# Kernel optimization log

Hardware: AMD Instinct MI355X
Metric: run time of the kernel (lower is better)

## Reference

```python
import jax, jax.numpy as jnp
import numpy as np

BN_EPS = 1e-5
N_NODES, N_EDGES, D_IN, HID = 100000, 1600000, 64, 128


def _bn(x, g, b, m, v):
    # BatchNorm1d in eval mode: running stats
    return (x - m) * jax.lax.rsqrt(v + BN_EPS) * g + b


def _gin_agg(x, edge_index, eps):
    # PyG GINConv aggregation: out[dst] = (1+eps)*x[dst] + sum_{src->dst} x[src]
    src, dst = edge_index[0], edge_index[1]
    s = jax.ops.segment_sum(x[src], dst, num_segments=x.shape[0])
    return (1.0 + eps) * x + s


def setup_inputs() -> dict:
    key = jax.random.key(0)
    ks = jax.random.split(key, 24)
    sc = 0.05
    d = {
        'x': jax.random.normal(ks[0], (N_NODES, D_IN), dtype=jnp.float32),
        'edge_index': jax.random.randint(ks[1], (2, N_EDGES), 0, N_NODES, dtype=jnp.int64),
        'eps1': jnp.zeros((), jnp.float32),
        'W1a': jax.random.normal(ks[2], (D_IN, HID), jnp.float32) * sc,
        'b1a': jnp.zeros((HID,), jnp.float32),
        'W1b': jax.random.normal(ks[3], (HID, HID), jnp.float32) * sc,
        'b1b': jnp.zeros((HID,), jnp.float32),
        'g1': jnp.ones((HID,), jnp.float32), 'be1': jnp.zeros((HID,), jnp.float32),
        'm1': jnp.zeros((HID,), jnp.float32), 'v1': jnp.ones((HID,), jnp.float32),
        'eps2': jnp.zeros((), jnp.float32),
        'W2a': jax.random.normal(ks[4], (HID, HID), jnp.float32) * sc,
        'b2a': jnp.zeros((HID,), jnp.float32),
        'g2': jnp.ones((HID,), jnp.float32), 'be2': jnp.zeros((HID,), jnp.float32),
        'm2': jnp.zeros((HID,), jnp.float32), 'v2': jnp.ones((HID,), jnp.float32),
        'eps3': jnp.zeros((), jnp.float32),
        'W3a': jax.random.normal(ks[5], (HID, HID), jnp.float32) * sc,
        'b3a': jnp.zeros((HID,), jnp.float32),
        'W3b': jax.random.normal(ks[6], (HID, HID), jnp.float32) * sc,
        'b3b': jnp.zeros((HID,), jnp.float32),
        'g3': jnp.ones((HID,), jnp.float32), 'be3': jnp.zeros((HID,), jnp.float32),
        'm3': jnp.zeros((HID,), jnp.float32), 'v3': jnp.ones((HID,), jnp.float32),
        'Wl': jax.random.normal(ks[7], (HID, HID), jnp.float32) * sc,
        'bl': jnp.zeros((HID,), jnp.float32),
        'Wf': jax.random.normal(ks[8], (HID, 1), jnp.float32) * sc,
        'bf': jnp.zeros((1,), jnp.float32),
    }
    return d


def reference(x, edge_index, eps1, W1a, b1a, W1b, b1b, g1, be1, m1, v1,
              eps2, W2a, b2a, g2, be2, m2, v2,
              eps3, W3a, b3a, W3b, b3b, g3, be3, m3, v3,
              Wl, bl, Wf, bf):
    # GINConv 1: agg -> Linear(64,128) ReLU -> Linear(128,128) ReLU -> BN
    h = _gin_agg(x, edge_index, eps1)
    h = jax.nn.relu(h @ W1a + b1a)
    h = jax.nn.relu(h @ W1b + b1b)
    h = _bn(h, g1, be1, m1, v1)
    # GINConv 2: agg -> Linear ReLU -> BN
    h = _gin_agg(h, edge_index, eps2)
    h = jax.nn.relu(h @ W2a + b2a)
    h = _bn(h, g2, be2, m2, v2)
    # GINConv 3: agg -> Linear ReLU -> Linear ReLU -> BN
    h = _gin_agg(h, edge_index, eps3)
    h = jax.nn.relu(h @ W3a + b3a)
    h = jax.nn.relu(h @ W3b + b3b)
    h = _bn(h, g3, be3, m3, v3)
    # head: lin1 + ReLU (dropout identity in eval), fc, squeeze
    h = jax.nn.relu(h @ Wl + bl)
    out = (h @ Wf + bf).squeeze(-1)  # [N]
    return out
```

## Files before the change

kernel.cpp:

```cpp
#include <hip/hip_runtime.h>


constexpr int NN  = 100000;
constexpr int NE  = 1600000;
constexpr int DIN = 64;
constexpr int HID = 128;

constexpr int BSH   = 9;
constexpr int NBUCK = 196;
constexpr int NBLK  = 200;
constexpr int CHUNK = 8000;

typedef __attribute__((ext_vector_type(4))) float f32x4;
typedef __attribute__((ext_vector_type(8))) short bf16x8;
typedef __attribute__((ext_vector_type(8))) unsigned short u16x8;

__device__ __forceinline__ short f2bf(float f) {
    union { float f; unsigned u; } x; x.f = f;
    unsigned r = x.u + 0x7fffu + ((x.u >> 16) & 1u);
    return (short)(r >> 16);
}
__device__ __forceinline__ float bf2f(short s) {
    union { unsigned u; float f; } x; x.u = ((unsigned)(unsigned short)s) << 16;
    return x.f;
}

__device__ __forceinline__ void wave_lds_fence() {
    __builtin_amdgcn_sched_barrier(0);
    asm volatile("s_waitcnt lgkmcnt(0)" ::: "memory");
    __builtin_amdgcn_sched_barrier(0);
}

__global__ __launch_bounds__(256)
void bhist_kernel(const int* __restrict__ eidx, int* __restrict__ bcnt,
                  int* __restrict__ pbase) {
    __shared__ int lh[NBUCK];
    int b = blockIdx.x;
    for (int i = threadIdx.x; i < NBUCK; i += 256) lh[i] = 0;
    __syncthreads();
    int e0 = b * CHUNK;
    for (int i = threadIdx.x; i < CHUNK; i += 256)
        atomicAdd(&lh[eidx[NE + e0 + i] >> BSH], 1);
    __syncthreads();
    for (int i = threadIdx.x; i < NBUCK; i += 256)
        pbase[b * NBUCK + i] = atomicAdd(&bcnt[i], lh[i]);
}

__global__ void bscan_kernel(const int* __restrict__ bcnt, int* __restrict__ bbase,
                             int* __restrict__ offs) {
    __shared__ int lds[256];
    int t = threadIdx.x;
    int v = (t < NBUCK) ? bcnt[t] : 0;
    lds[t] = v; __syncthreads();
    #pragma unroll
    for (int o = 1; o < 256; o <<= 1) {
        int x = (t >= o) ? lds[t - o] : 0;
        __syncthreads();
        lds[t] += x;
        __syncthreads();
    }
    if (t < NBUCK) bbase[t] = lds[t] - v;
    if (t == 0) { bbase[NBUCK] = NE; offs[NN] = NE; }
}

__global__ __launch_bounds__(256)
void part_kernel(const int* __restrict__ eidx, const int* __restrict__ bbase,
                 const int* __restrict__ pbase, int2* __restrict__ tmp) {
    __shared__ int lh[NBUCK], lofs[NBUCK], lcnt[NBUCK], gb[NBUCK];
    __shared__ int sb[256];
    __shared__ int2 lp[CHUNK];
    int b = blockIdx.x;
    int t = threadIdx.x;
    for (int i = t; i < NBUCK; i += 256) { lh[i] = 0; lcnt[i] = 0; }
    __syncthreads();
    int e0 = b * CHUNK;
    for (int i = t; i < CHUNK; i += 256)
        atomicAdd(&lh[eidx[NE + e0 + i] >> BSH], 1);
    __syncthreads();
    {
        int v = (t < NBUCK) ? lh[t] : 0;
        sb[t] = v; __syncthreads();
        #pragma unroll
        for (int o = 1; o < 256; o <<= 1) {
            int x = (t >= o) ? sb[t - o] : 0;
            __syncthreads();
            sb[t] += x;
            __syncthreads();
        }
        if (t < NBUCK) {
            lofs[t] = sb[t] - v;
            gb[t]   = bbase[t] + pbase[b * NBUCK + t];
        }
    }
    __syncthreads();
    for (int i = t; i < CHUNK; i += 256) {
        int s = eidx[e0 + i], d = eidx[NE + e0 + i];
        int bk = d >> BSH;
        int r = atomicAdd(&lcnt[bk], 1);
        lp[lofs[bk] + r] = int2{s, d};
    }
    __syncthreads();
    for (int i = t; i < CHUNK; i += 256) {
        int2 p = lp[i];
        int bk = p.y >> BSH;
        tmp[gb[bk] + (i - lofs[bk])] = p;
    }
}

__global__ __launch_bounds__(512)
void bsort_kernel(const int* __restrict__ bbase, const int2* __restrict__ tmp,
                  int* __restrict__ offs, int* __restrict__ esrc) {
    __shared__ int h[512], lo[512], cnt[512];
    int bk = blockIdx.x;
    int n0 = bk << BSH;
    int lo0 = bbase[bk], hi0 = bbase[bk + 1];
    int t = threadIdx.x;
    h[t] = 0; cnt[t] = 0;
    __syncthreads();
    for (int i = lo0 + t; i < hi0; i += 512)
        atomicAdd(&h[tmp[i].y - n0], 1);
    __syncthreads();
    int v = h[t];
    lo[t] = v; __syncthreads();
    #pragma unroll
    for (int o = 1; o < 512; o <<= 1) {
        int x = (t >= o) ? lo[t - o] : 0;
        __syncthreads();
        lo[t] += x;
        __syncthreads();
    }
    int excl = lo[t] - v;
    __syncthreads();
    lo[t] = excl;
    __syncthreads();
    if (n0 + t < NN) offs[n0 + t] = lo0 + excl;
    for (int i = lo0 + t; i < hi0; i += 512) {
        int2 p = tmp[i];
        int ld = p.y - n0;
        int r = atomicAdd(&cnt[ld], 1);
        esrc[lo0 + lo[ld] + r] = p.x;
    }
}

__global__ void cvt_kernel(const float* __restrict__ x, unsigned short* __restrict__ xb) {
    int i = blockIdx.x * 256 + threadIdx.x;
    if (i >= NN * DIN / 8) return;
    const f32x4* p = (const f32x4*)x + (size_t)i * 2;
    f32x4 v0 = p[0], v1 = p[1];
    u16x8 o;
    #pragma unroll
    for (int j = 0; j < 4; ++j) {
        o[j]     = (unsigned short)f2bf(v0[j]);
        o[j + 4] = (unsigned short)f2bf(v1[j]);
    }
    ((u16x8*)xb)[i] = o;
}

template<int D>
__global__ __launch_bounds__(256)
void aggb_kernel(const float* __restrict__ hf, const unsigned short* __restrict__ hb,
                 const int* __restrict__ offs, const int* __restrict__ esrc,
                 const float* __restrict__ epsp, float* __restrict__ out) {
    constexpr int TPN = D / 8;
    int node = blockIdx.x * (256 / TPN) + threadIdx.x / TPN;
    int f    = threadIdx.x % TPN;
    if (node >= NN) return;
    const u16x8* h8 = (const u16x8*)hb;
    float eps = 1.0f + *epsp;

    const float* hrow = hf + (size_t)node * D + f * 8;
    f32x4 a0 = *(const f32x4*)hrow * eps;
    f32x4 a1 = *(const f32x4*)(hrow + 4) * eps;
    f32x4 b0 = (f32x4)0.f, b1 = (f32x4)0.f;

    union { unsigned u; float fv; } cvt;
    auto acc8 = [&](u16x8 t, f32x4& x0, f32x4& x1) {
        #pragma unroll
        for (int j = 0; j < 4; ++j) { cvt.u = ((unsigned)t[j]) << 16;     x0[j] += cvt.fv; }
        #pragma unroll
        for (int j = 0; j < 4; ++j) { cvt.u = ((unsigned)t[j + 4]) << 16; x1[j] += cvt.fv; }
    };

    int k = offs[node], k1 = offs[node + 1];
    for (; k + 8 <= k1; k += 8) {
        int s0 = esrc[k+0], s1 = esrc[k+1], s2 = esrc[k+2], s3 = esrc[k+3];
        int s4 = esrc[k+4], s5 = esrc[k+5], s6 = esrc[k+6], s7 = esrc[k+7];
        u16x8 t0 = h8[(size_t)s0*TPN+f], t1 = h8[(size_t)s1*TPN+f];
        u16x8 t2 = h8[(size_t)s2*TPN+f], t3 = h8[(size_t)s3*TPN+f];
        u16x8 t4 = h8[(size_t)s4*TPN+f], t5 = h8[(size_t)s5*TPN+f];
        u16x8 t6 = h8[(size_t)s6*TPN+f], t7 = h8[(size_t)s7*TPN+f];
        acc8(t0, a0, a1); acc8(t1, b0, b1); acc8(t2, a0, a1); acc8(t3, b0, b1);
        acc8(t4, a0, a1); acc8(t5, b0, b1); acc8(t6, a0, a1); acc8(t7, b0, b1);
    }
    for (; k + 2 <= k1; k += 2) {
        u16x8 t0 = h8[(size_t)esrc[k]*TPN+f];
        u16x8 t1 = h8[(size_t)esrc[k+1]*TPN+f];
        acc8(t0, a0, a1); acc8(t1, b0, b1);
    }
    if (k < k1) acc8(h8[(size_t)esrc[k]*TPN+f], a0, a1);

    float* orow = out + (size_t)node * D + f * 8;
    *(f32x4*)orow       = a0 + b0;
    *(f32x4*)(orow + 4) = a1 + b1;
}

__global__ void packall_kernel(const float* __restrict__ W1a, const float* __restrict__ W1b,
                               const float* __restrict__ W2a, const float* __restrict__ W3a,
                               const float* __restrict__ W3b, const float* __restrict__ Wl,
                               short* P1a, short* P1b, short* P2a,
                               short* P3a, short* P3b, short* Pl) {
    const float* W; short* P; int K;
    switch (blockIdx.y) {
        case 0: W = W1a; P = P1a; K = 64;  break;
        case 1: W = W1b; P = P1b; K = 128; break;
        case 2: W = W2a; P = P2a; K = 128; break;
        case 3: W = W3a; P = P3a; K = 128; break;
        case 4: W = W3b; P = P3b; K = 128; break;
        default: W = Wl; P = Pl;  K = 128; break;
    }
    int T = (K / 32) * 8 * 64;
    int idx = blockIdx.x * 256 + threadIdx.x;
    if (idx >= T) return;
    int c  = idx >> 9;
    int nt = (idx >> 6) & 7;
    int l  = idx & 63;
    int col   = nt * 16 + (l & 15);
    int kbase = c * 32 + (l >> 4) * 8;
    bf16x8 hi, lo;
    #pragma unroll
    for (int j = 0; j < 8; ++j) {
        float w = W[(kbase + j) * HID + col];
        short h = f2bf(w);
        hi[j] = h;
        lo[j] = f2bf(w - bf2f(h));
    }
    *(bf16x8*)&P[(size_t)idx * 8]       = hi;
    *(bf16x8*)&P[(size_t)(T + idx) * 8] = lo;
}

__global__ __launch_bounds__(512)
void gemm_bn_kernel(const float* __restrict__ A, const short* __restrict__ P,
                    const float* __restrict__ bias,
                    const float* __restrict__ g, const float* __restrict__ be,
                    const float* __restrict__ m, const float* __restrict__ v,
                    float* __restrict__ out, unsigned short* __restrict__ hbout, int M) {
    constexpr int NCH = 4;
    constexpr int T   = NCH * 8 * 64;
    __shared__ short wlds[2 * T * 8];

    const int tid  = threadIdx.x;
    const int wid  = tid >> 6;
    const int lane = tid & 63;

    for (int i = tid; i < 2 * T; i += 512)
        ((bf16x8*)wlds)[i] = ((const bf16x8*)P)[i];
    __syncthreads();

    const int rlo  = lane & 15;
    const int kgrp = lane >> 4;
    const int row  = blockIdx.x * 128 + wid * 16 + rlo;
    const int r    = row < M ? row : M - 1;
    const float* arow = A + (size_t)r * 128 + kgrp * 8;

    f32x4 acc[8];
    #pragma unroll
    for (int i = 0; i < 8; ++i) acc[i] = (f32x4)0.0f;

    #pragma unroll
    for (int c = 0; c < NCH; ++c) {
        f32x4 a0 = *(const f32x4*)(arow + c * 32);
        f32x4 a1 = *(const f32x4*)(arow + c * 32 + 4);
        bf16x8 ah, al;
        #pragma unroll
        for (int j = 0; j < 4; ++j) {
            short h0 = f2bf(a0[j]);
            short h1 = f2bf(a1[j]);
            ah[j]     = h0;
            ah[j + 4] = h1;
            al[j]     = f2bf(a0[j] - bf2f(h0));
            al[j + 4] = f2bf(a1[j] - bf2f(h1));
        }
        #pragma unroll
        for (int nt = 0; nt < 8; ++nt) {
            int fi = ((c * 8) + nt) * 64 + lane;
            bf16x8 wh = *(bf16x8*)&wlds[(size_t)fi * 8];
            bf16x8 wl = *(bf16x8*)&wlds[(size_t)(T + fi) * 8];
            acc[nt] = __builtin_amdgcn_mfma_f32_16x16x32_bf16(ah, wh, acc[nt], 0, 0, 0);
            acc[nt] = __builtin_amdgcn_mfma_f32_16x16x32_bf16(al, wh, acc[nt], 0, 0, 0);
            acc[nt] = __builtin_amdgcn_mfma_f32_16x16x32_bf16(ah, wl, acc[nt], 0, 0, 0);
        }
    }

    #pragma unroll
    for (int nt = 0; nt < 8; ++nt) {
        int col  = nt * 16 + rlo;
        float bb = bias[col];
        float sv = g[col] * rsqrtf(v[col] + 1e-5f);
        float tv = be[col] - m[col] * sv;
        #pragma unroll
        for (int jj = 0; jj < 4; ++jj) {
            int rr = blockIdx.x * 128 + wid * 16 + kgrp * 4 + jj;
            float val = fmaxf(acc[nt][jj] + bb, 0.f) * sv + tv;
            if (rr < M) {
                out[(size_t)rr * 128 + col] = val;
                hbout[(size_t)rr * 128 + col] = (unsigned short)f2bf(val);
            }
        }
    }
}

template<int K1>
__global__ __launch_bounds__(128)
void fused2_kernel(const float* __restrict__ A,
                   const short* __restrict__ P1, const float* __restrict__ bias1,
                   const short* __restrict__ P2, const float* __restrict__ bias2,
                   const float* __restrict__ g, const float* __restrict__ be,
                   const float* __restrict__ m, const float* __restrict__ v,
                   float* __restrict__ out, unsigned short* __restrict__ hbout, int M) {
    constexpr int NCH1 = K1 / 32;
    constexpr int T1   = NCH1 * 8 * 64;
    constexpr int T2   = 4 * 8 * 64;
    constexpr int LDW  = 136;
    __shared__ short h1hi[64 * LDW];
    __shared__ short h1lo[64 * LDW];

    const int tid  = threadIdx.x;
    const int wid  = tid >> 6;
    const int lane = tid & 63;
    const int rlo  = lane & 15;
    const int kgrp = lane >> 4;

    const int rowA = blockIdx.x * 64 + wid * 16 + rlo;
    const int rowB = rowA + 32;
    const int rA   = rowA < M ? rowA : M - 1;
    const int rB   = rowB < M ? rowB : M - 1;
    const float* arowA = A + (size_t)rA * K1 + kgrp * 8;
    const float* arowB = A + (size_t)rB * K1 + kgrp * 8;

    const bf16x8* P1v = (const bf16x8*)P1;
    const bf16x8* P2v = (const bf16x8*)P2;

    f32x4 accA[8], accB[8];
    #pragma unroll
    for (int i = 0; i < 8; ++i) { accA[i] = (f32x4)0.0f; accB[i] = (f32x4)0.0f; }

    #pragma unroll
    for (int c = 0; c < NCH1; ++c) {
        f32x4 aA0 = *(const f32x4*)(arowA + c * 32);
        f32x4 aA1 = *(const f32x4*)(arowA + c * 32 + 4);
        f32x4 aB0 = *(const f32x4*)(arowB + c * 32);
        f32x4 aB1 = *(const f32x4*)(arowB + c * 32 + 4);
        bf16x8 ahA, alA, ahB, alB;
        #pragma unroll
        for (int j = 0; j < 4; ++j) {
            short h;
            h = f2bf(aA0[j]); ahA[j]   = h; alA[j]   = f2bf(aA0[j] - bf2f(h));
            h = f2bf(aA1[j]); ahA[j+4] = h; alA[j+4] = f2bf(aA1[j] - bf2f(h));
            h = f2bf(aB0[j]); ahB[j]   = h; alB[j]   = f2bf(aB0[j] - bf2f(h));
            h = f2bf(aB1[j]); ahB[j+4] = h; alB[j+4] = f2bf(aB1[j] - bf2f(h));
        }
        #pragma unroll
        for (int nt = 0; nt < 8; ++nt) {
            int fi = ((c * 8) + nt) * 64 + lane;
            bf16x8 wh = P1v[fi];
            bf16x8 wl = P1v[T1 + fi];
            accA[nt] = __builtin_amdgcn_mfma_f32_16x16x32_bf16(ahA, wh, accA[nt], 0, 0, 0);
            accA[nt] = __builtin_amdgcn_mfma_f32_16x16x32_bf16(alA, wh, accA[nt], 0, 0, 0);
            accA[nt] = __builtin_amdgcn_mfma_f32_16x16x32_bf16(ahA, wl, accA[nt], 0, 0, 0);
            accB[nt] = __builtin_amdgcn_mfma_f32_16x16x32_bf16(ahB, wh, accB[nt], 0, 0, 0);
            accB[nt] = __builtin_amdgcn_mfma_f32_16x16x32_bf16(alB, wh, accB[nt], 0, 0, 0);
            accB[nt] = __builtin_amdgcn_mfma_f32_16x16x32_bf16(ahB, wl, accB[nt], 0, 0, 0);
        }
    }

    #pragma unroll
    for (int nt = 0; nt < 8; ++nt) {
        int col  = nt * 16 + rlo;
        float bb = bias1[col];
        #pragma unroll
        for (int jj = 0; jj < 4; ++jj) {
            int lrA = wid * 16 + kgrp * 4 + jj;
            float vA = fmaxf(accA[nt][jj] + bb, 0.f);
            short hA = f2bf(vA);
            h1hi[lrA * LDW + col] = hA;
            h1lo[lrA * LDW + col] = f2bf(vA - bf2f(hA));
            int lrB = lrA + 32;
            float vB = fmaxf(accB[nt][jj] + bb, 0.f);
            short hB = f2bf(vB);
            h1hi[lrB * LDW + col] = hB;
            h1lo[lrB * LDW + col] = f2bf(vB - bf2f(hB));
        }
    }
    wave_lds_fence();

    #pragma unroll
    for (int i = 0; i < 8; ++i) { accA[i] = (f32x4)0.0f; accB[i] = (f32x4)0.0f; }
    const int lrA2 = wid * 16 + rlo;
    const int lrB2 = lrA2 + 32;
    #pragma unroll
    for (int c = 0; c < 4; ++c) {
        bf16x8 ahA = *(bf16x8*)&h1hi[lrA2 * LDW + c * 32 + kgrp * 8];
        bf16x8 alA = *(bf16x8*)&h1lo[lrA2 * LDW + c * 32 + kgrp * 8];
        bf16x8 ahB = *(bf16x8*)&h1hi[lrB2 * LDW + c * 32 + kgrp * 8];
        bf16x8 alB = *(bf16x8*)&h1lo[lrB2 * LDW + c * 32 + kgrp * 8];
        #pragma unroll
        for (int nt = 0; nt < 8; ++nt) {
            int fi = ((c * 8) + nt) * 64 + lane;
            bf16x8 wh = P2v[fi];
            bf16x8 wl = P2v[T2 + fi];
            accA[nt] = __builtin_amdgcn_mfma_f32_16x16x32_bf16(ahA, wh, accA[nt], 0, 0, 0);
            accA[nt] = __builtin_amdgcn_mfma_f32_16x16x32_bf16(alA, wh, accA[nt], 0, 0, 0);
            accA[nt] = __builtin_amdgcn_mfma_f32_16x16x32_bf16(ahA, wl, accA[nt], 0, 0, 0);
            accB[nt] = __builtin_amdgcn_mfma_f32_16x16x32_bf16(ahB, wh, accB[nt], 0, 0, 0);
            accB[nt] = __builtin_amdgcn_mfma_f32_16x16x32_bf16(alB, wh, accB[nt], 0, 0, 0);
            accB[nt] = __builtin_amdgcn_mfma_f32_16x16x32_bf16(ahB, wl, accB[nt], 0, 0, 0);
        }
    }

    #pragma unroll
    for (int nt = 0; nt < 8; ++nt) {
        int col  = nt * 16 + rlo;
        float bb = bias2[col];
        float sv = g[col] * rsqrtf(v[col] + 1e-5f);
        float tv = be[col] - m[col] * sv;
        #pragma unroll
        for (int jj = 0; jj < 4; ++jj) {
            int rrA = blockIdx.x * 64 + wid * 16 + kgrp * 4 + jj;
            float vA = fmaxf(accA[nt][jj] + bb, 0.f) * sv + tv;
            if (rrA < M) {
                out[(size_t)rrA * 128 + col] = vA;
                hbout[(size_t)rrA * 128 + col] = (unsigned short)f2bf(vA);
            }
            int rrB = rrA + 32;
            float vB = fmaxf(accB[nt][jj] + bb, 0.f) * sv + tv;
            if (rrB < M) {
                out[(size_t)rrB * 128 + col] = vB;
                hbout[(size_t)rrB * 128 + col] = (unsigned short)f2bf(vB);
            }
        }
    }
}

__global__ __launch_bounds__(128)
void fused3_kernel(const float* __restrict__ A,
                   const short* __restrict__ P1, const float* __restrict__ bias1,
                   const short* __restrict__ P2, const float* __restrict__ bias2,
                   const float* __restrict__ g, const float* __restrict__ be,
                   const float* __restrict__ m, const float* __restrict__ v,
                   const short* __restrict__ Pl, const float* __restrict__ bl,
                   const float* __restrict__ Wf, const float* __restrict__ bf,
                   float* __restrict__ out, int M) {
    constexpr int T  = 4 * 8 * 64;
    constexpr int LDW = 136;
    __shared__ short h1hi[64 * LDW];
    __shared__ short h1lo[64 * LDW];

    const int tid  = threadIdx.x;
    const int wid  = tid >> 6;
    const int lane = tid & 63;
    const int rlo  = lane & 15;
    const int kgrp = lane >> 4;

    const int rowA = blockIdx.x * 64 + wid * 16 + rlo;
    const int rowB = rowA + 32;
    const int rA   = rowA < M ? rowA : M - 1;
    const int rB   = rowB < M ? rowB : M - 1;
    const float* arowA = A + (size_t)rA * 128 + kgrp * 8;
    const float* arowB = A + (size_t)rB * 128 + kgrp * 8;

    const bf16x8* P1v = (const bf16x8*)P1;
    const bf16x8* P2v = (const bf16x8*)P2;
    const bf16x8* Plv = (const bf16x8*)Pl;

    f32x4 accA[8], accB[8];
    #pragma unroll
    for (int i = 0; i < 8; ++i) { accA[i] = (f32x4)0.0f; accB[i] = (f32x4)0.0f; }

    #pragma unroll
    for (int c = 0; c < 4; ++c) {
        f32x4 aA0 = *(const f32x4*)(arowA + c * 32);
        f32x4 aA1 = *(const f32x4*)(arowA + c * 32 + 4);
        f32x4 aB0 = *(const f32x4*)(arowB + c * 32);
        f32x4 aB1 = *(const f32x4*)(arowB + c * 32 + 4);
        bf16x8 ahA, alA, ahB, alB;
        #pragma unroll
        for (int j = 0; j < 4; ++j) {
            short h;
            h = f2bf(aA0[j]); ahA[j]   = h; alA[j]   = f2bf(aA0[j] - bf2f(h));
            h = f2bf(aA1[j]); ahA[j+4] = h; alA[j+4] = f2bf(aA1[j] - bf2f(h));
            h = f2bf(aB0[j]); ahB[j]   = h; alB[j]   = f2bf(aB0[j] - bf2f(h));
            h = f2bf(aB1[j]); ahB[j+4] = h; alB[j+4] = f2bf(aB1[j] - bf2f(h));
        }
        #pragma unroll
        for (int nt = 0; nt < 8; ++nt) {
            int fi = ((c * 8) + nt) * 64 + lane;
            bf16x8 wh = P1v[fi];
            bf16x8 wl = P1v[T + fi];
            accA[nt] = __builtin_amdgcn_mfma_f32_16x16x32_bf16(ahA, wh, accA[nt], 0, 0, 0);
            accA[nt] = __builtin_amdgcn_mfma_f32_16x16x32_bf16(alA, wh, accA[nt], 0, 0, 0);
            accA[nt] = __builtin_amdgcn_mfma_f32_16x16x32_bf16(ahA, wl, accA[nt], 0, 0, 0);
            accB[nt] = __builtin_amdgcn_mfma_f32_16x16x32_bf16(ahB, wh, accB[nt], 0, 0, 0);
            accB[nt] = __builtin_amdgcn_mfma_f32_16x16x32_bf16(alB, wh, accB[nt], 0, 0, 0);
            accB[nt] = __builtin_amdgcn_mfma_f32_16x16x32_bf16(ahB, wl, accB[nt], 0, 0, 0);
        }
    }
    #pragma unroll
    for (int nt = 0; nt < 8; ++nt) {
        int col  = nt * 16 + rlo;
        float bb = bias1[col];
        #pragma unroll
        for (int jj = 0; jj < 4; ++jj) {
            int lrA = wid * 16 + kgrp * 4 + jj;
            float vA = fmaxf(accA[nt][jj] + bb, 0.f);
            short hA = f2bf(vA);
            h1hi[lrA * LDW + col] = hA;
            h1lo[lrA * LDW + col] = f2bf(vA - bf2f(hA));
            int lrB = lrA + 32;
            float vB = fmaxf(accB[nt][jj] + bb, 0.f);
            short hB = f2bf(vB);
            h1hi[lrB * LDW + col] = hB;
            h1lo[lrB * LDW + col] = f2bf(vB - bf2f(hB));
        }
    }
    wave_lds_fence();

    const int lrA2 = wid * 16 + rlo;
    const int lrB2 = lrA2 + 32;
    #pragma unroll
    for (int i = 0; i < 8; ++i) { accA[i] = (f32x4)0.0f; accB[i] = (f32x4)0.0f; }
    #pragma unroll
    for (int c = 0; c < 4; ++c) {
        bf16x8 ahA = *(bf16x8*)&h1hi[lrA2 * LDW + c * 32 + kgrp * 8];
        bf16x8 alA = *(bf16x8*)&h1lo[lrA2 * LDW + c * 32 + kgrp * 8];
        bf16x8 ahB = *(bf16x8*)&h1hi[lrB2 * LDW + c * 32 + kgrp * 8];
        bf16x8 alB = *(bf16x8*)&h1lo[lrB2 * LDW + c * 32 + kgrp * 8];
        #pragma unroll
        for (int nt = 0; nt < 8; ++nt) {
            int fi = ((c * 8) + nt) * 64 + lane;
            bf16x8 wh = P2v[fi];
            bf16x8 wl = P2v[T + fi];
            accA[nt] = __builtin_amdgcn_mfma_f32_16x16x32_bf16(ahA, wh, accA[nt], 0, 0, 0);
            accA[nt] = __builtin_amdgcn_mfma_f32_16x16x32_bf16(alA, wh, accA[nt], 0, 0, 0);
            accA[nt] = __builtin_amdgcn_mfma_f32_16x16x32_bf16(ahA, wl, accA[nt], 0, 0, 0);
            accB[nt] = __builtin_amdgcn_mfma_f32_16x16x32_bf16(ahB, wh, accB[nt], 0, 0, 0);
            accB[nt] = __builtin_amdgcn_mfma_f32_16x16x32_bf16(alB, wh, accB[nt], 0, 0, 0);
            accB[nt] = __builtin_amdgcn_mfma_f32_16x16x32_bf16(ahB, wl, accB[nt], 0, 0, 0);
        }
    }
    wave_lds_fence();
    #pragma unroll
    for (int nt = 0; nt < 8; ++nt) {
        int col  = nt * 16 + rlo;
        float bb = bias2[col];
        float sv = g[col] * rsqrtf(v[col] + 1e-5f);
        float tv = be[col] - m[col] * sv;
        #pragma unroll
        for (int jj = 0; jj < 4; ++jj) {
            int lrA = wid * 16 + kgrp * 4 + jj;
            float vA = fmaxf(accA[nt][jj] + bb, 0.f) * sv + tv;
            short hA = f2bf(vA);
            h1hi[lrA * LDW + col] = hA;
            h1lo[lrA * LDW + col] = f2bf(vA - bf2f(hA));
            int lrB = lrA + 32;
            float vB = fmaxf(accB[nt][jj] + bb, 0.f) * sv + tv;
            short hB = f2bf(vB);
            h1hi[lrB * LDW + col] = hB;
            h1lo[lrB * LDW + col] = f2bf(vB - bf2f(hB));
        }
    }
    wave_lds_fence();

    #pragma unroll
    for (int i = 0; i < 8; ++i) { accA[i] = (f32x4)0.0f; accB[i] = (f32x4)0.0f; }
    #pragma unroll
    for (int c = 0; c < 4; ++c) {
        bf16x8 ahA = *(bf16x8*)&h1hi[lrA2 * LDW + c * 32 + kgrp * 8];
        bf16x8 alA = *(bf16x8*)&h1lo[lrA2 * LDW + c * 32 + kgrp * 8];
        bf16x8 ahB = *(bf16x8*)&h1hi[lrB2 * LDW + c * 32 + kgrp * 8];
        bf16x8 alB = *(bf16x8*)&h1lo[lrB2 * LDW + c * 32 + kgrp * 8];
        #pragma unroll
        for (int nt = 0; nt < 8; ++nt) {
            int fi = ((c * 8) + nt) * 64 + lane;
            bf16x8 wh = Plv[fi];
            bf16x8 wl = Plv[T + fi];
            accA[nt] = __builtin_amdgcn_mfma_f32_16x16x32_bf16(ahA, wh, accA[nt], 0, 0, 0);
            accA[nt] = __builtin_amdgcn_mfma_f32_16x16x32_bf16(alA, wh, accA[nt], 0, 0, 0);
            accA[nt] = __builtin_amdgcn_mfma_f32_16x16x32_bf16(ahA, wl, accA[nt], 0, 0, 0);
            accB[nt] = __builtin_amdgcn_mfma_f32_16x16x32_bf16(ahB, wh, accB[nt], 0, 0, 0);
            accB[nt] = __builtin_amdgcn_mfma_f32_16x16x32_bf16(alB, wh, accB[nt], 0, 0, 0);
            accB[nt] = __builtin_amdgcn_mfma_f32_16x16x32_bf16(ahB, wl, accB[nt], 0, 0, 0);
        }
    }
    float pA0 = 0, pA1 = 0, pA2 = 0, pA3 = 0;
    float pB0 = 0, pB1 = 0, pB2 = 0, pB3 = 0;
    #pragma unroll
    for (int nt = 0; nt < 8; ++nt) {
        int col  = nt * 16 + rlo;
        float bb = bl[col];
        float wv = Wf[col];
        pA0 += fmaxf(accA[nt][0] + bb, 0.f) * wv;
        pA1 += fmaxf(accA[nt][1] + bb, 0.f) * wv;
        pA2 += fmaxf(accA[nt][2] + bb, 0.f) * wv;
        pA3 += fmaxf(accA[nt][3] + bb, 0.f) * wv;
        pB0 += fmaxf(accB[nt][0] + bb, 0.f) * wv;
        pB1 += fmaxf(accB[nt][1] + bb, 0.f) * wv;
        pB2 += fmaxf(accB[nt][2] + bb, 0.f) * wv;
        pB3 += fmaxf(accB[nt][3] + bb, 0.f) * wv;
    }
    #pragma unroll
    for (int o = 1; o < 16; o <<= 1) {
        pA0 += __shfl_xor(pA0, o); pA1 += __shfl_xor(pA1, o);
        pA2 += __shfl_xor(pA2, o); pA3 += __shfl_xor(pA3, o);
        pB0 += __shfl_xor(pB0, o); pB1 += __shfl_xor(pB1, o);
        pB2 += __shfl_xor(pB2, o); pB3 += __shfl_xor(pB3, o);
    }
    if (rlo == 0) {
        int rbase = blockIdx.x * 64 + wid * 16 + kgrp * 4;
        float bfv = bf[0];
        if (rbase + 0 < M) out[rbase + 0] = pA0 + bfv;
        if (rbase + 1 < M) out[rbase + 1] = pA1 + bfv;
        if (rbase + 2 < M) out[rbase + 2] = pA2 + bfv;
        if (rbase + 3 < M) out[rbase + 3] = pA3 + bfv;
        int rb2 = rbase + 32;
        if (rb2 + 0 < M) out[rb2 + 0] = pB0 + bfv;
        if (rb2 + 1 < M) out[rb2 + 1] = pB1 + bfv;
        if (rb2 + 2 < M) out[rb2 + 2] = pB2 + bfv;
        if (rb2 + 3 < M) out[rb2 + 3] = pB3 + bfv;
    }
}

extern "C" void kernel_launch(void* const* d_in, const int* in_sizes, int n_in,
                              void* d_out, int out_size, void* d_ws, size_t ws_size,
                              hipStream_t stream) {
    const float* x    = (const float*)d_in[0];
    const int*   eidx = (const int*)d_in[1];
    const float* eps1 = (const float*)d_in[2];
    const float* W1a  = (const float*)d_in[3];
    const float* b1a  = (const float*)d_in[4];
    const float* W1b  = (const float*)d_in[5];
    const float* b1b  = (const float*)d_in[6];
    const float* g1   = (const float*)d_in[7];
    const float* be1  = (const float*)d_in[8];
    const float* m1   = (const float*)d_in[9];
    const float* v1   = (const float*)d_in[10];
    const float* eps2 = (const float*)d_in[11];
    const float* W2a  = (const float*)d_in[12];
    const float* b2a  = (const float*)d_in[13];
    const float* g2   = (const float*)d_in[14];
    const float* be2  = (const float*)d_in[15];
    const float* m2   = (const float*)d_in[16];
    const float* v2   = (const float*)d_in[17];
    const float* eps3 = (const float*)d_in[18];
    const float* W3a  = (const float*)d_in[19];
    const float* b3a  = (const float*)d_in[20];
    const float* W3b  = (const float*)d_in[21];
    const float* b3b  = (const float*)d_in[22];
    const float* g3   = (const float*)d_in[23];
    const float* be3  = (const float*)d_in[24];
    const float* m3   = (const float*)d_in[25];
    const float* v3   = (const float*)d_in[26];
    const float* Wl   = (const float*)d_in[27];
    const float* bl   = (const float*)d_in[28];
    const float* Wf   = (const float*)d_in[29];
    const float* bfp  = (const float*)d_in[30];

    char* ws = (char*)d_ws;
    size_t off = 0;
    auto alloc = [&](size_t bytes) -> void* {
        off = (off + 255) & ~(size_t)255;
        void* p = ws + off;
        off += bytes;
        return p;
    };

    float*          bufA = (float*)alloc((size_t)NN * 128 * 4);
    float*          bufB = (float*)alloc((size_t)NN * 128 * 4);
    unsigned short* hb   = (unsigned short*)alloc((size_t)NN * 128 * 2);
    int*   offs   = (int*)alloc((size_t)(NN + 1) * 4);
    int*   esrc   = (int*)alloc((size_t)NE * 4);
    int*   bcnt   = (int*)alloc((size_t)NBUCK * 4);
    int*   bbase  = (int*)alloc((size_t)(NBUCK + 1) * 4);
    int*   pbase  = (int*)alloc((size_t)NBLK * NBUCK * 4);
    short* P1a    = (short*)alloc((size_t)2 * DIN * HID * 2);
    short* P1b    = (short*)alloc((size_t)2 * HID * HID * 2);
    short* P2a    = (short*)alloc((size_t)2 * HID * HID * 2);
    short* P3a    = (short*)alloc((size_t)2 * HID * HID * 2);
    short* P3b    = (short*)alloc((size_t)2 * HID * HID * 2);
    short* Pl     = (short*)alloc((size_t)2 * HID * HID * 2);
    int2*  tmp    = (int2*)bufA;

    const int GRID_G    = (NN + 127) / 128;
    const int GRID_F    = (NN + 63) / 64;
    const int GRID_A64  = (NN + 31) / 32;
    const int GRID_A128 = (NN + 15) / 16;

    hipMemsetAsync(bcnt, 0, (size_t)NBUCK * 4, stream);
    bhist_kernel<<<NBLK, 256, 0, stream>>>(eidx, bcnt, pbase);
    bscan_kernel<<<1, 256, 0, stream>>>(bcnt, bbase, offs);
    part_kernel<<<NBLK, 256, 0, stream>>>(eidx, bbase, pbase, tmp);
    bsort_kernel<<<NBUCK, 512, 0, stream>>>(bbase, tmp, offs, esrc);

    {
        dim3 grid(8, 6);
        packall_kernel<<<grid, 256, 0, stream>>>(W1a, W1b, W2a, W3a, W3b, Wl,
                                                 P1a, P1b, P2a, P3a, P3b, Pl);
    }
    cvt_kernel<<<(NN * DIN / 8 + 255) / 256, 256, 0, stream>>>(x, hb);

    aggb_kernel<64><<<GRID_A64, 256, 0, stream>>>(x, hb, offs, esrc, eps1, bufA);
    fused2_kernel<64><<<GRID_F, 128, 0, stream>>>(bufA, P1a, b1a, P1b, b1b,
                                                  g1, be1, m1, v1, bufB, hb, NN);
    aggb_kernel<128><<<GRID_A128, 256, 0, stream>>>(bufB, hb, offs, esrc, eps2, bufA);
    gemm_bn_kernel<<<GRID_G, 512, 0, stream>>>(bufA, P2a, b2a, g2, be2, m2, v2,
                                               bufB, hb, NN);
    aggb_kernel<128><<<GRID_A128, 256, 0, stream>>>(bufB, hb, offs, esrc, eps3, bufA);
    fused3_kernel<<<GRID_F, 128, 0, stream>>>(bufA, P3a, b3a, P3b, b3b,
                                              g3, be3, m3, v3, Pl, bl, Wf, bfp,
                                              (float*)d_out, NN);
}
```

Baseline: 368.4 us.

## Pad CSR rows to multiples of eight and sort nodes by degree for aggregation

Each node's neighbor list is padded to a multiple of eight, using a dummy zero row at index NN, so the aggregation loop runs only the 8-way unrolled body with no remainder loops. Nodes are also bucketed by padded degree through a histogram, scan and scatter, and aggregation threads walk them in that order to balance the work within each wave. The cost is three extra small preprocessing kernels, a larger padded edge array, and output writes and self-row reads that become scattered because nodes are no longer visited in index order. A separate bf16 buffer for x is added so the padding row is kept apart for the 64-wide and 128-wide feature layouts.

```diff
diff --git a/kernel.cpp b/kernel.cpp
--- a/kernel.cpp
+++ b/kernel.cpp
@@ -10,6 +10,8 @@
 constexpr int NBUCK = 196;
 constexpr int NBLK  = 200;
 constexpr int CHUNK = 8000;
+constexpr int PADB  = 4096;
+constexpr int DBINS = 128;
 
 typedef __attribute__((ext_vector_type(4))) float f32x4;
 typedef __attribute__((ext_vector_type(8))) short bf16x8;
@@ -46,8 +48,7 @@
         pbase[b * NBUCK + i] = atomicAdd(&bcnt[i], lh[i]);
 }
 
-__global__ void bscan_kernel(const int* __restrict__ bcnt, int* __restrict__ bbase,
-                             int* __restrict__ offs) {
+__global__ void bscan_kernel(const int* __restrict__ bcnt, int* __restrict__ bbase) {
     __shared__ int lds[256];
     int t = threadIdx.x;
     int v = (t < NBUCK) ? bcnt[t] : 0;
@@ -60,7 +61,7 @@
         __syncthreads();
     }
     if (t < NBUCK) bbase[t] = lds[t] - v;
-    if (t == 0) { bbase[NBUCK] = NE; offs[NN] = NE; }
+    if (t == 0) bbase[NBUCK] = NE;
 }
 
 __global__ __launch_bounds__(256)
@@ -109,19 +110,22 @@
 
 __global__ __launch_bounds__(512)
 void bsort_kernel(const int* __restrict__ bbase, const int2* __restrict__ tmp,
-                  int* __restrict__ offs, int* __restrict__ esrc) {
+                  int* __restrict__ offs, int* __restrict__ pcnt,
+                  int* __restrict__ esrc) {
     __shared__ int h[512], lo[512], cnt[512];
     int bk = blockIdx.x;
     int n0 = bk << BSH;
     int lo0 = bbase[bk], hi0 = bbase[bk + 1];
+    int padlo = lo0 + PADB * bk;
     int t = threadIdx.x;
     h[t] = 0; cnt[t] = 0;
     __syncthreads();
     for (int i = lo0 + t; i < hi0; i += 512)
         atomicAdd(&h[tmp[i].y - n0], 1);
     __syncthreads();
-    int v = h[t];
-    lo[t] = v; __syncthreads();
+    int d  = h[t];
+    int pd = (d + 7) & ~7;
+    lo[t] = pd; __syncthreads();
     #pragma unroll
     for (int o = 1; o < 512; o <<= 1) {
         int x = (t >= o) ? lo[t - o] : 0;
@@ -129,16 +133,73 @@
         lo[t] += x;
         __syncthreads();
     }
-    int excl = lo[t] - v;
+    int excl = lo[t] - pd;
     __syncthreads();
     lo[t] = excl;
     __syncthreads();
-    if (n0 + t < NN) offs[n0 + t] = lo0 + excl;
+    if (n0 + t < NN) {
+        offs[n0 + t] = padlo + excl;
+        pcnt[n0 + t] = pd;
+    }
     for (int i = lo0 + t; i < hi0; i += 512) {
         int2 p = tmp[i];
         int ld = p.y - n0;
         int r = atomicAdd(&cnt[ld], 1);
-        esrc[lo0 + lo[ld] + r] = p.x;
+        esrc[padlo + lo[ld] + r] = p.x;
+    }
+    for (int j = d; j < pd; ++j)
+        esrc[padlo + excl + j] = NN;
+}
+
+__global__ __launch_bounds__(256)
+void dhist_kernel(const int* __restrict__ pcnt, int* __restrict__ dh) {
+    __shared__ int lh[DBINS];
+    for (int i = threadIdx.x; i < DBINS; i += 256) lh[i] = 0;
+    __syncthreads();
+    int n = blockIdx.x * 256 + threadIdx.x;
+    if (n < NN) {
+        int b = pcnt[n] >> 3; if (b > DBINS - 1) b = DBINS - 1;
+        atomicAdd(&lh[b], 1);
+    }
+    __syncthreads();
+    for (int i = threadIdx.x; i < DBINS; i += 256)
+        if (lh[i]) atomicAdd(&dh[i], lh[i]);
+}
+
+__global__ void dscan_kernel(int* __restrict__ dh, int* __restrict__ dcur) {
+    __shared__ int l[DBINS];
+    int t = threadIdx.x;
+    int v = dh[t];
+    l[t] = v; __syncthreads();
+    #pragma unroll
+    for (int o = 1; o < DBINS; o <<= 1) {
+        int x = (t >= o) ? l[t - o] : 0;
+        __syncthreads();
+        l[t] += x;
+        __syncthreads();
+    }
+    dcur[t] = l[t] - v;
+}
+
+__global__ __launch_bounds__(256)
+void dscatter_kernel(const int* __restrict__ pcnt, int* __restrict__ dcur,
+                     int* __restrict__ order) {
+    __shared__ int lh[DBINS], gbase[DBINS], lcnt[DBINS];
+    for (int i = threadIdx.x; i < DBINS; i += 256) { lh[i] = 0; lcnt[i] = 0; }
+    __syncthreads();
+    int n = blockIdx.x * 256 + threadIdx.x;
+    int b = -1;
+    if (n < NN) {
+        b = pcnt[n] >> 3; if (b > DBINS - 1) b = DBINS - 1;
+        atomicAdd(&lh[b], 1);
+    }
+    __syncthreads();
+    for (int i = threadIdx.x; i < DBINS; i += 256)
+        gbase[i] = lh[i] ? atomicAdd(&dcur[i], lh[i]) : 0;
+    __syncthreads();
+    if (n < NN) {
+        int r = atomicAdd(&lcnt[b], 1);
+        order[gbase[b] + r] = n;
     }
 }
 
@@ -159,12 +220,14 @@
 template<int D>
 __global__ __launch_bounds__(256)
 void aggb_kernel(const float* __restrict__ hf, const unsigned short* __restrict__ hb,
-                 const int* __restrict__ offs, const int* __restrict__ esrc,
+                 const int* __restrict__ offs, const int* __restrict__ pcnt,
+                 const int* __restrict__ order, const int* __restrict__ esrc,
                  const float* __restrict__ epsp, float* __restrict__ out) {
     constexpr int TPN = D / 8;
-    int node = blockIdx.x * (256 / TPN) + threadIdx.x / TPN;
+    int gidx = blockIdx.x * (256 / TPN) + threadIdx.x / TPN;
     int f    = threadIdx.x % TPN;
-    if (node >= NN) return;
+    if (gidx >= NN) return;
+    int node = order[gidx];
     const u16x8* h8 = (const u16x8*)hb;
     float eps = 1.0f + *epsp;
 
@@ -181,8 +244,9 @@
         for (int j = 0; j < 4; ++j) { cvt.u = ((unsigned)t[j + 4]) << 16; x1[j] += cvt.fv; }
     };
 
-    int k = offs[node], k1 = offs[node + 1];
-    for (; k + 8 <= k1; k += 8) {
+    int k  = offs[node];
+    int k1 = k + pcnt[node];
+    for (; k < k1; k += 8) {
         int s0 = esrc[k+0], s1 = esrc[k+1], s2 = esrc[k+2], s3 = esrc[k+3];
         int s4 = esrc[k+4], s5 = esrc[k+5], s6 = esrc[k+6], s7 = esrc[k+7];
         u16x8 t0 = h8[(size_t)s0*TPN+f], t1 = h8[(size_t)s1*TPN+f];
@@ -192,12 +256,6 @@
         acc8(t0, a0, a1); acc8(t1, b0, b1); acc8(t2, a0, a1); acc8(t3, b0, b1);
         acc8(t4, a0, a1); acc8(t5, b0, b1); acc8(t6, a0, a1); acc8(t7, b0, b1);
     }
-    for (; k + 2 <= k1; k += 2) {
-        u16x8 t0 = h8[(size_t)esrc[k]*TPN+f];
-        u16x8 t1 = h8[(size_t)esrc[k+1]*TPN+f];
-        acc8(t0, a0, a1); acc8(t1, b0, b1);
-    }
-    if (k < k1) acc8(h8[(size_t)esrc[k]*TPN+f], a0, a1);
 
     float* orow = out + (size_t)node * D + f * 8;
     *(f32x4*)orow       = a0 + b0;
@@ -673,14 +731,21 @@
         return p;
     };
 
+    const int ESRC_N = NE + PADB * NBUCK;
+
     float*          bufA = (float*)alloc((size_t)NN * 128 * 4);
     float*          bufB = (float*)alloc((size_t)NN * 128 * 4);
-    unsigned short* hb   = (unsigned short*)alloc((size_t)NN * 128 * 2);
-    int*   offs   = (int*)alloc((size_t)(NN + 1) * 4);
-    int*   esrc   = (int*)alloc((size_t)NE * 4);
+    unsigned short* hb   = (unsigned short*)alloc((size_t)(NN + 1) * 128 * 2);
+    unsigned short* xbh  = (unsigned short*)alloc((size_t)(NN + 1) * DIN * 2);
+    int*   offs   = (int*)alloc((size_t)NN * 4);
+    int*   pcnt   = (int*)alloc((size_t)NN * 4);
+    int*   order  = (int*)alloc((size_t)NN * 4);
+    int*   esrc   = (int*)alloc((size_t)ESRC_N * 4);
     int*   bcnt   = (int*)alloc((size_t)NBUCK * 4);
     int*   bbase  = (int*)alloc((size_t)(NBUCK + 1) * 4);
     int*   pbase  = (int*)alloc((size_t)NBLK * NBUCK * 4);
+    int*   dh     = (int*)alloc((size_t)DBINS * 4);
+    int*   dcur   = (int*)alloc((size_t)DBINS * 4);
     short* P1a    = (short*)alloc((size_t)2 * DIN * HID * 2);
     short* P1b    = (short*)alloc((size_t)2 * HID * HID * 2);
     short* P2a    = (short*)alloc((size_t)2 * HID * HID * 2);
@@ -693,27 +758,38 @@
     const int GRID_F    = (NN + 63) / 64;
     const int GRID_A64  = (NN + 31) / 32;
     const int GRID_A128 = (NN + 15) / 16;
+    const int GRID_N    = (NN + 255) / 256;
 
     hipMemsetAsync(bcnt, 0, (size_t)NBUCK * 4, stream);
+    hipMemsetAsync(dh, 0, (size_t)DBINS * 4, stream);
+    hipMemsetAsync(hb + (size_t)NN * 128, 0, 128 * 2, stream);
+    hipMemsetAsync(xbh + (size_t)NN * DIN, 0, DIN * 2, stream);
     bhist_kernel<<<NBLK, 256, 0, stream>>>(eidx, bcnt, pbase);
-    bscan_kernel<<<1, 256, 0, stream>>>(bcnt, bbase, offs);
+    bscan_kernel<<<1, 256, 0, stream>>>(bcnt, bbase);
     part_kernel<<<NBLK, 256, 0, stream>>>(eidx, bbase, pbase, tmp);
-    bsort_kernel<<<NBUCK, 512, 0, stream>>>(bbase, tmp, offs, esrc);
+    bsort_kernel<<<NBUCK, 512, 0, stream>>>(bbase, tmp, offs, pcnt, esrc);
+
+    dhist_kernel<<<GRID_N, 256, 0, stream>>>(pcnt, dh);
+    dscan_kernel<<<1, DBINS, 0, stream>>>(dh, dcur);
+    dscatter_kernel<<<GRID_N, 256, 0, stream>>>(pcnt, dcur, order);
 
     {
         dim3 grid(8, 6);
         packall_kernel<<<grid, 256, 0, stream>>>(W1a, W1b, W2a, W3a, W3b, Wl,
                                                  P1a, P1b, P2a, P3a, P3b, Pl);
     }
-    cvt_kernel<<<(NN * DIN / 8 + 255) / 256, 256, 0, stream>>>(x, hb);
-
-    aggb_kernel<64><<<GRID_A64, 256, 0, stream>>>(x, hb, offs, esrc, eps1, bufA);
+    cvt_kernel<<<(NN * DIN / 8 + 255) / 256, 256, 0, stream>>>(x, xbh);
+
+    aggb_kernel<64><<<GRID_A64, 256, 0, stream>>>(x, xbh, offs, pcnt, order,
+                                                  esrc, eps1, bufA);
     fused2_kernel<64><<<GRID_F, 128, 0, stream>>>(bufA, P1a, b1a, P1b, b1b,
                                                   g1, be1, m1, v1, bufB, hb, NN);
-    aggb_kernel<128><<<GRID_A128, 256, 0, stream>>>(bufB, hb, offs, esrc, eps2, bufA);
+    aggb_kernel<128><<<GRID_A128, 256, 0, stream>>>(bufB, hb, offs, pcnt, order,
+                                                    esrc, eps2, bufA);
     gemm_bn_kernel<<<GRID_G, 512, 0, stream>>>(bufA, P2a, b2a, g2, be2, m2, v2,
                                                bufB, hb, NN);
-    aggb_kernel<128><<<GRID_A128, 256, 0, stream>>>(bufB, hb, offs, esrc, eps3, bufA);
+    aggb_kernel<128><<<GRID_A128, 256, 0, stream>>>(bufB, hb, offs, pcnt, order,
+                                                    esrc, eps3, bufA);
     fused3_kernel<<<GRID_F, 128, 0, stream>>>(bufA, P3a, b3a, P3b, b3b,
                                               g3, be3, m3, v3, Pl, bl, Wf, bfp,
                                               (float*)d_out, NN);
```

Measured after the change: 392.3 us. +6.5%, slower.
